# Kernel tuning notes

Measured on AMD Instinct MI355X. Metric: run time of the kernel, lower is better.

The kernel has to match this reference:

```python
import jax, jax.numpy as jnp
import numpy as np

K = 3   # 4D kernel size
P = 1   # padding (all 4 dims)
S = 1   # stride (all 4 dims)
DIL = 1 # dilation

def setup_inputs() -> dict:
    key = jax.random.key(0)
    k1, k2, k3 = jax.random.split(key, 3)
    x = jax.random.normal(k1, (2, 8, 16, 40, 40, 40), dtype=jnp.float32)
    # K separate Conv3d layers: weight[i] has shape [C_o, C_i, K, K, K]
    weight = jax.random.normal(k2, (K, 32, 8, K, K, K), dtype=jnp.float32) * 0.05
    bias = jax.random.normal(k3, (K, 32), dtype=jnp.float32) * 0.05
    return {"x": x, "weight": weight, "bias": bias}

def reference(x, weight, bias):
    # x: [B, C_i, T, D, H, W]; weight: [K, C_o, C_i, K, K, K]; bias: [K, C_o]
    B, Ci, T, D, H, W = x.shape
    Co = weight.shape[1]
    O = (T + 2 * P - K) // S + 1
    # Fold temporal frames into the batch dim and all K conv3d filters into
    # the output-channel dim -> a single conv3d replaces K*T launches.
    x2 = jnp.transpose(x, (0, 2, 1, 3, 4, 5)).reshape(B * T, Ci, D, H, W)
    w = weight.reshape(K * Co, Ci, K, K, K)
    y = jax.lax.conv_general_dilated(
        x2, w,
        window_strides=(S, S, S),
        padding=[(P, P)] * 3,
        rhs_dilation=(DIL, DIL, DIL),
        dimension_numbers=("NCDHW", "OIDHW", "NCDHW"),
    )  # [B*T, K*Co, Dp, Hp, Wp]
    Dp, Hp, Wp = y.shape[-3:]
    y = y.reshape(B, T, K, Co, Dp, Hp, Wp)
    # bias is added per Conv3d call, i.e. once per contributing (i, j) pair
    y = y + bias[None, None, :, :, None, None, None]
    # Temporal accumulation: out[o] = sum_i y[j = o*S + i - P, i] (skip OOB j),
    # implemented via zero-padding (padded frames contribute nothing, incl. bias).
    y_pad = jnp.pad(y, ((0, 0), (P, P), (0, 0), (0, 0), (0, 0), (0, 0), (0, 0)))
    idx = jnp.arange(O)[:, None] * S + jnp.arange(K)[None, :]  # [O, K] indices into padded T
    gathered = y_pad[:, idx, jnp.arange(K)[None, :]]  # [B, O, K, Co, Dp, Hp, Wp]
    out = gathered.sum(axis=2)  # [B, O, Co, Dp, Hp, Wp]
    return jnp.transpose(out, (0, 2, 1, 3, 4, 5))  # [B, Co, O, Dp, Hp, Wp]
```

## Files before the change

kernel.cpp:

```cpp
#include <hip/hip_runtime.h>


typedef unsigned int u32;
typedef unsigned short u16;
typedef __attribute__((ext_vector_type(8))) short short8;
typedef __attribute__((ext_vector_type(4))) float f32x4;

#define XT_OFF_BYTES 65536

__device__ __forceinline__ u32 bf16r(float f) {
    u32 u = __float_as_uint(f);
    return (u + 0x7FFFu + ((u >> 16) & 1u)) >> 16;
}

__device__ __forceinline__ void glds16(const void* g, void* l) {
    __builtin_amdgcn_global_load_lds((const __attribute__((address_space(1))) u32*)g,
                                     (__attribute__((address_space(3))) u32*)l, 16, 0, 0);
}

__global__ __launch_bounds__(256) void prep_xw(const float* __restrict__ x,
                                               const float* __restrict__ wgt,
                                               u16* __restrict__ xtp,
                                               u16* __restrict__ wf) {
    if (blockIdx.x >= 9261) {
        const int idx = (blockIdx.x - 9261) * 256 + threadIdx.x;
        const int kt = idx / 7168;
        const int r  = idx - kt * 7168;
        const int s2 = r >> 9;
        const int l  = (r >> 3) & 63;
        const int j  = r & 7;
        const int co = (s2 & 1) * 16 + (l & 15);
        const int k  = (s2 >> 1) * 32 + (l >> 4) * 8 + j;
        u32 v = 0;
        if (k < 216) {
            const int ci = k & 7;
            const int combo = k >> 3;
            const int kd = combo / 9;
            const int r9 = combo - kd * 9;
            const int kh = r9 / 3;
            const int kw = r9 - kh * 3;
            v = bf16r(wgt[((kt * 32 + co) * 8 + ci) * 27 + kd * 9 + kh * 3 + kw]);
        }
        wf[idx] = (u16)v;
        return;
    }
    const int c = blockIdx.x * 256 + threadIdx.x;
    int wp = c % 42;
    int tmp = c / 42;
    const int hp = tmp % 42; tmp /= 42;
    const int dp = tmp % 42; tmp /= 42;
    const int t  = tmp % 16;
    const int b  = tmp / 16;
    const int wa = wp - 1, ha = hp - 1, da = dp - 1;
    u32 q0 = 0, q1 = 0, q2 = 0, q3 = 0;
    if ((unsigned)wa < 40u && (unsigned)ha < 40u && (unsigned)da < 40u) {
        const float* xp = x + ((b * 8) * 16 + t) * 64000 + da * 1600 + ha * 40 + wa;
        float v0 = xp[0];
        float v1 = xp[1024000];
        float v2 = xp[2048000];
        float v3 = xp[3072000];
        float v4 = xp[4096000];
        float v5 = xp[5120000];
        float v6 = xp[6144000];
        float v7 = xp[7168000];
        q0 = bf16r(v0) | (bf16r(v1) << 16);
        q1 = bf16r(v2) | (bf16r(v3) << 16);
        q2 = bf16r(v4) | (bf16r(v5) << 16);
        q3 = bf16r(v6) | (bf16r(v7) << 16);
    }
    uint4 q; q.x = q0; q.y = q1; q.z = q2; q.w = q3;
    *(uint4*)(xtp + (size_t)c * 8) = q;
}

__global__ __launch_bounds__(256, 3) void conv4d_mfma(
    const u16* __restrict__ xtp, const u16* __restrict__ wf,
    const float* __restrict__ bias, float* __restrict__ out)
{
    __shared__ __align__(16) u16 sHalo[2][10080];
    __shared__ float sBsum[32];

    const int tid  = threadIdx.x;
    const int lane = tid & 63;
    const int wid  = tid >> 6;
    const int bi   = blockIdx.x;
    const int h0   = (bi % 5) * 8;
    const int d    = (bi / 5) % 40;
    const int o    = (bi / 200) % 16;
    const int b    = bi / 3200;

    if (tid < 32) {
        float s = 0.f;
        for (int kt = 0; kt < 3; ++kt) {
            int t = o + kt - 1;
            if ((unsigned)t < 16u) s += bias[kt * 32 + tid];
        }
        sBsum[tid] = s;
    }

    const int quad = lane >> 4;
    const int nl   = lane & 15;

    int lb[5];
#pragma unroll
    for (int tl = 0; tl < 5; ++tl) {
        int n = wid * 80 + tl * 16 + nl;
        int hh = n / 40;
        int ww = n - hh * 40;
        lb[tl] = (hh * 42 + ww) * 16;
    }

    int offs7[7];
#pragma unroll
    for (int s = 0; s < 7; ++s) {
        const int c0 = 4 * s;
        int O0 = (c0+0 < 27) ? (((c0+0)/9)*420 + (((c0+0)%9)/3)*42 + ((c0+0)%3)) * 16 : 0;
        int O1 = (c0+1 < 27) ? (((c0+1)/9)*420 + (((c0+1)%9)/3)*42 + ((c0+1)%3)) * 16 : 0;
        int O2 = (c0+2 < 27) ? (((c0+2)/9)*420 + (((c0+2)%9)/3)*42 + ((c0+2)%3)) * 16 : 0;
        int O3 = (c0+3 < 27) ? (((c0+3)/9)*420 + (((c0+3)%9)/3)*42 + ((c0+3)%3)) * 16 : 0;
        offs7[s] = (quad & 2) ? ((quad & 1) ? O3 : O2) : ((quad & 1) ? O1 : O0);
    }

    const f32x4 zero = {0.f, 0.f, 0.f, 0.f};
    f32x4 acc[2][5];
#pragma unroll
    for (int mt = 0; mt < 2; ++mt)
#pragma unroll
        for (int tl = 0; tl < 5; ++tl) acc[mt][tl] = zero;

    const int kt_lo = (o == 0)  ? 1 : 0;
    const int kt_hi = (o == 15) ? 1 : 2;
    const int nkt   = kt_hi - kt_lo + 1;

#define STAGE(KT, DST)                                                                   \
    {                                                                                    \
        const int t_ = o + (KT) - 1;                                                     \
        const u16* gbase_ = xtp + (size_t)(b * 16 + t_) * 592704 + h0 * 336;             \
        const int jw_ = wid * 315;                                                       \
        _Pragma("unroll")                                                                \
        for (int i_ = 0; i_ < 5; ++i_) {                                                 \
            const int j_ = jw_ + i_ * 64 + lane;                                         \
            if (i_ < 4 || lane < 59) {                                                   \
                const int dpp_ = j_ / 420;                                               \
                const int r_ = j_ - dpp_ * 420;                                          \
                glds16(gbase_ + (d + dpp_) * 14112 + r_ * 8,                             \
                       (char*)(DST) + (jw_ + i_ * 64) * 16);                             \
            }                                                                            \
        }                                                                                \
    }

#define COMPUTE(KT, BUF)                                                                 \
    {                                                                                    \
        const u16* wfk_ = wf + (KT) * 7168;                                              \
        _Pragma("unroll")                                                                \
        for (int s_ = 0; s_ < 7; ++s_) {                                                 \
            const short8 a0_ = *(const short8*)(wfk_ + s_ * 1024 + lane * 8);            \
            const short8 a1_ = *(const short8*)(wfk_ + s_ * 1024 + 512 + lane * 8);      \
            const int off_ = offs7[s_];                                                  \
            _Pragma("unroll")                                                            \
            for (int tl_ = 0; tl_ < 5; ++tl_) {                                          \
                const short8 bf_ = *(const short8*)((const char*)(BUF) + lb[tl_] + off_);\
                acc[0][tl_] = __builtin_amdgcn_mfma_f32_16x16x32_bf16(a0_, bf_, acc[0][tl_], 0, 0, 0); \
                acc[1][tl_] = __builtin_amdgcn_mfma_f32_16x16x32_bf16(a1_, bf_, acc[1][tl_], 0, 0, 0); \
            }                                                                            \
        }                                                                                \
    }

    STAGE(kt_lo, sHalo[0]);
    __syncthreads();

    STAGE(kt_lo + 1, sHalo[1]);
    COMPUTE(kt_lo, sHalo[0]);
    __syncthreads();

    if (nkt == 3) {
        STAGE(kt_lo + 2, sHalo[0]);
        COMPUTE(kt_lo + 1, sHalo[1]);
        __syncthreads();
        COMPUTE(kt_lo + 2, sHalo[0]);
    } else {
        COMPUTE(kt_lo + 1, sHalo[1]);
    }

    const int coB = quad * 4;
    float bs[2][4];
#pragma unroll
    for (int mt = 0; mt < 2; ++mt)
#pragma unroll
        for (int reg = 0; reg < 4; ++reg) bs[mt][reg] = sBsum[mt * 16 + coB + reg];

#pragma unroll
    for (int mt = 0; mt < 2; ++mt)
#pragma unroll
        for (int tl = 0; tl < 5; ++tl) {
            int n = wid * 80 + tl * 16 + nl;
            int hh = n / 40;
            int ww = n - hh * 40;
            const size_t base = (size_t)(((b * 32 + mt * 16 + coB) * 16 + o)) * 64000
                              + d * 1600 + (h0 + hh) * 40 + ww;
#pragma unroll
            for (int reg = 0; reg < 4; ++reg)
                out[base + (size_t)reg * 1024000] = acc[mt][tl][reg] + bs[mt][reg];
        }
}

extern "C" void kernel_launch(void* const* d_in, const int* in_sizes, int n_in,
                              void* d_out, int out_size, void* d_ws, size_t ws_size,
                              hipStream_t stream)
{
    const float* x    = (const float*)d_in[0];
    const float* wgt  = (const float*)d_in[1];
    const float* bias = (const float*)d_in[2];
    float* out = (float*)d_out;
    u16* wfbuf = (u16*)d_ws;
    u16* xtp   = (u16*)((char*)d_ws + XT_OFF_BYTES);
    (void)in_sizes; (void)n_in; (void)out_size; (void)ws_size;

    prep_xw<<<dim3(9345), dim3(256), 0, stream>>>(x, wgt, xtp, wfbuf);
    conv4d_mfma<<<dim3(6400), dim3(256), 0, stream>>>(xtp, wfbuf, bias, out);
}
```

Measured before the change: 371.3 us.

## Share staged input frames across two adjacent output frames per block

Each block now computes two adjacent temporal outputs with 8 waves, one group of 4 waves per output. It loads the 4 needed input frame halos into LDS once up front, so the two overlapping frames are reused instead of being fetched by separate blocks. This cuts global/L2 traffic for the halo by about a third. In exchange, the double-buffered load/compute overlap is removed: all loads finish before a single barrier. LDS per block doubles, which may reduce occupancy.

```diff
diff --git a/kernel.cpp b/kernel.cpp
--- a/kernel.cpp
+++ b/kernel.cpp
@@ -72,38 +72,44 @@
     *(uint4*)(xtp + (size_t)c * 8) = q;
 }
 
-__global__ __launch_bounds__(256, 3) void conv4d_mfma(
+__global__ __launch_bounds__(512, 4) void conv4d_mfma(
     const u16* __restrict__ xtp, const u16* __restrict__ wf,
     const float* __restrict__ bias, float* __restrict__ out)
 {
-    __shared__ __align__(16) u16 sHalo[2][10080];
-    __shared__ float sBsum[32];
+    __shared__ __align__(16) u16 sHalo[4][10080];
+    __shared__ float sBsum[2][32];
 
     const int tid  = threadIdx.x;
     const int lane = tid & 63;
     const int wid  = tid >> 6;
+    const int g    = wid >> 2;
+    const int w4   = wid & 3;
     const int bi   = blockIdx.x;
     const int h0   = (bi % 5) * 8;
     const int d    = (bi / 5) % 40;
-    const int o    = (bi / 200) % 16;
-    const int b    = bi / 3200;
-
-    if (tid < 32) {
+    const int ob   = ((bi / 200) & 7) * 2;
+    const int b    = bi / 1600;
+
+    if (tid < 64) {
+        const int gg = tid >> 5;
+        const int co = tid & 31;
+        const int oo = ob + gg;
         float s = 0.f;
         for (int kt = 0; kt < 3; ++kt) {
-            int t = o + kt - 1;
-            if ((unsigned)t < 16u) s += bias[kt * 32 + tid];
-        }
-        sBsum[tid] = s;
+            int t = oo + kt - 1;
+            if ((unsigned)t < 16u) s += bias[kt * 32 + co];
+        }
+        sBsum[gg][co] = s;
     }
 
     const int quad = lane >> 4;
     const int nl   = lane & 15;
+    const int o    = ob + g;
 
     int lb[5];
 #pragma unroll
     for (int tl = 0; tl < 5; ++tl) {
-        int n = wid * 80 + tl * 16 + nl;
+        int n = w4 * 80 + tl * 16 + nl;
         int hh = n / 40;
         int ww = n - hh * 40;
         lb[tl] = (hh * 42 + ww) * 16;
@@ -120,6 +126,25 @@
         offs7[s] = (quad & 2) ? ((quad & 1) ? O3 : O2) : ((quad & 1) ? O1 : O0);
     }
 
+    {
+        const u16* gb = xtp + (size_t)(b * 16) * 592704 + h0 * 336 + d * 14112;
+#pragma unroll
+        for (int i = 0; i < 10; ++i) {
+            const int j = i * 512 + tid;
+            if (i < 9 || j < 5040) {
+                const int pl  = j / 1260;
+                const int r1  = j - pl * 1260;
+                const int t   = ob - 1 + pl;
+                if ((unsigned)t < 16u) {
+                    const int dpp = r1 / 420;
+                    const int row = r1 - dpp * 420;
+                    glds16(gb + (size_t)t * 592704 + dpp * 14112 + row * 8,
+                           (char*)sHalo + (size_t)(i * 512 + wid * 64) * 16);
+                }
+            }
+        }
+    }
+
     const f32x4 zero = {0.f, 0.f, 0.f, 0.f};
     f32x4 acc[2][5];
 #pragma unroll
@@ -127,26 +152,7 @@
 #pragma unroll
         for (int tl = 0; tl < 5; ++tl) acc[mt][tl] = zero;
 
-    const int kt_lo = (o == 0)  ? 1 : 0;
-    const int kt_hi = (o == 15) ? 1 : 2;
-    const int nkt   = kt_hi - kt_lo + 1;
-
-#define STAGE(KT, DST)                                                                   \
-    {                                                                                    \
-        const int t_ = o + (KT) - 1;                                                     \
-        const u16* gbase_ = xtp + (size_t)(b * 16 + t_) * 592704 + h0 * 336;             \
-        const int jw_ = wid * 315;                                                       \
-        _Pragma("unroll")                                                                \
-        for (int i_ = 0; i_ < 5; ++i_) {                                                 \
-            const int j_ = jw_ + i_ * 64 + lane;                                         \
-            if (i_ < 4 || lane < 59) {                                                   \
-                const int dpp_ = j_ / 420;                                               \
-                const int r_ = j_ - dpp_ * 420;                                          \
-                glds16(gbase_ + (d + dpp_) * 14112 + r_ * 8,                             \
-                       (char*)(DST) + (jw_ + i_ * 64) * 16);                             \
-            }                                                                            \
-        }                                                                                \
-    }
+    __syncthreads();
 
 #define COMPUTE(KT, BUF)                                                                 \
     {                                                                                    \
@@ -165,20 +171,11 @@
         }                                                                                \
     }
 
-    STAGE(kt_lo, sHalo[0]);
-    __syncthreads();
-
-    STAGE(kt_lo + 1, sHalo[1]);
-    COMPUTE(kt_lo, sHalo[0]);
-    __syncthreads();
-
-    if (nkt == 3) {
-        STAGE(kt_lo + 2, sHalo[0]);
-        COMPUTE(kt_lo + 1, sHalo[1]);
-        __syncthreads();
-        COMPUTE(kt_lo + 2, sHalo[0]);
-    } else {
-        COMPUTE(kt_lo + 1, sHalo[1]);
+#pragma unroll
+    for (int kt = 0; kt < 3; ++kt) {
+        if ((unsigned)(o + kt - 1) < 16u) {
+            COMPUTE(kt, sHalo[g + kt]);
+        }
     }
 
     const int coB = quad * 4;
@@ -186,13 +183,13 @@
 #pragma unroll
     for (int mt = 0; mt < 2; ++mt)
 #pragma unroll
-        for (int reg = 0; reg < 4; ++reg) bs[mt][reg] = sBsum[mt * 16 + coB + reg];
+        for (int reg = 0; reg < 4; ++reg) bs[mt][reg] = sBsum[g][mt * 16 + coB + reg];
 
 #pragma unroll
     for (int mt = 0; mt < 2; ++mt)
 #pragma unroll
         for (int tl = 0; tl < 5; ++tl) {
-            int n = wid * 80 + tl * 16 + nl;
+            int n = w4 * 80 + tl * 16 + nl;
             int hh = n / 40;
             int ww = n - hh * 40;
             const size_t base = (size_t)(((b * 32 + mt * 16 + coB) * 16 + o)) * 64000
@@ -216,5 +213,5 @@
     (void)in_sizes; (void)n_in; (void)out_size; (void)ws_size;
 
     prep_xw<<<dim3(9345), dim3(256), 0, stream>>>(x, wgt, xtp, wfbuf);
-    conv4d_mfma<<<dim3(6400), dim3(256), 0, stream>>>(xtp, wfbuf, bias, out);
-}
+    conv4d_mfma<<<dim3(3200), dim3(512), 0, stream>>>(xtp, wfbuf, bias, out);
+}
```

After: 365.3 us. About the same (-1.6%).
